# Kernel optimization log

Hardware: AMD Instinct MI355X
Metric: run time of the kernel (lower is better)

The kernel has to match this reference:

```python
import jax, jax.numpy as jnp
import numpy as np

B, N, NH, H = 32, 512, 4, 32      # batch, agents per group, heads, hidden per head
IN_DIM, OUT_DIM = 128, 128
BIG = 9.0e15
SQRT_DK = float(np.sqrt(H))


def setup_inputs() -> dict:
    key = jax.random.key(0)
    keys = iter(jax.random.split(key, 64))

    def nrm(shape, scale=0.05):
        return jax.random.normal(next(keys), shape, dtype=jnp.float32) * scale

    inp = {}
    inp["x0"] = jax.random.normal(next(keys), (B, N, IN_DIM), dtype=jnp.float32)
    inp["x1"] = jax.random.normal(next(keys), (B, N, IN_DIM), dtype=jnp.float32)
    for name in ("m00", "m01", "m10", "m11"):
        inp[name] = jax.random.randint(next(keys), (B, N, N), 0, 2, dtype=jnp.int32)
    # per-group q/k/v projections: Linear(in_dim, NH*H)
    for g in (0, 1):
        inp[f"wq{g}"] = nrm((IN_DIM, NH * H)); inp[f"bq{g}"] = nrm((NH * H,))
        inp[f"wk{g}"] = nrm((IN_DIM, NH * H)); inp[f"bk{g}"] = nrm((NH * H,))
        inp[f"wv{g}"] = nrm((IN_DIM, NH * H)); inp[f"bv{g}"] = nrm((NH * H,))
    # fc_outs[i][j]: Linear(NH*H, H)
    for i in (0, 1):
        for j in (0, 1):
            inp[f"wo{i}{j}"] = nrm((NH * H, H)); inp[f"bo{i}{j}"] = nrm((H,))
    # fc_out_final[i]: Linear(H * 2, out_dim)
    for g in (0, 1):
        inp[f"wf{g}"] = nrm((2 * H, OUT_DIM)); inp[f"bf{g}"] = nrm((OUT_DIM,))
    return inp


def _qkv(x, wq, bq, wk, bk, wv, bv):
    q = jax.nn.relu(x @ wq + bq)
    k = jax.nn.relu(x @ wk + bk)
    v = jax.nn.relu(x @ wv + bv)
    return q, k, v


def _split_heads(t):
    # [B, N, NH*H] -> [B, NH, N, H]; contiguous H-blocks == torch per-head slices
    return t.reshape(B, t.shape[1], NH, H).transpose(0, 2, 1, 3)


def _attend(q, k, v, mask, gate):
    qh, kh, vh = _split_heads(q), _split_heads(k), _split_heads(v)
    logits = jnp.einsum('bhqd,bhkd->bhqk', qh, kh) / SQRT_DK
    m = mask.astype(logits.dtype)[:, None]            # [B,1,Nq,Nk]
    w = jax.nn.softmax(logits * m - BIG * (1.0 - m), axis=-1)
    if gate:
        has = (mask.sum(axis=-1) > 0).astype(w.dtype)  # [B,Nq]
        w = w * has[:, None, :, None]
    out = jnp.einsum('bhqk,bhkd->bhqd', w, vh)
    # heads concatenated along feature dim (matches torch.cat of head slices)
    return out.transpose(0, 2, 1, 3).reshape(B, q.shape[1], NH * H)


def reference(x0, x1, m00, m01, m10, m11,
              wq0, bq0, wk0, bk0, wv0, bv0,
              wq1, bq1, wk1, bk1, wv1, bv1,
              wo00, bo00, wo01, bo01, wo10, bo10, wo11, bo11,
              wf0, bf0, wf1, bf1):
    q0, k0, v0 = _qkv(x0, wq0, bq0, wk0, bk0, wv0, bv0)
    q1, k1, v1 = _qkv(x1, wq1, bq1, wk1, bk1, wv1, bv1)
    inner0 = jax.nn.relu(_attend(q0, k0, v0, m00, gate=False) @ wo00 + bo00)
    inner1 = jax.nn.relu(_attend(q1, k1, v1, m11, gate=False) @ wo11 + bo11)
    inter0 = jax.nn.relu(_attend(q0, k1, v1, m01, gate=True) @ wo01 + bo01)
    inter1 = jax.nn.relu(_attend(q1, k0, v0, m10, gate=True) @ wo10 + bo10)
    out0 = jnp.concatenate([inner0, inter0], axis=-1) @ wf0 + bf0
    out1 = jnp.concatenate([inner1, inter1], axis=-1) @ wf1 + bf1
    return (out0, out1)
```

## Files before the change

### kernel.cpp

```cpp
#include <hip/hip_runtime.h>

#define B_    32
#define N_    512
#define D_    128
#define ROWS  (B_ * N_)
#define SCALE_ 0.17677669529663687f

typedef __bf16 bf16x8 __attribute__((ext_vector_type(8)));
typedef __bf16 bf16x4 __attribute__((ext_vector_type(4)));
typedef float  f32x4  __attribute__((ext_vector_type(4)));

static __device__ __forceinline__ f32x4 mfma16(bf16x8 a, bf16x8 b, f32x4 c) {
  return __builtin_amdgcn_mfma_f32_16x16x32_bf16(a, b, c, 0, 0, 0);
}

__global__ __launch_bounds__(256) void prep_kernel(
    const int* __restrict__ m00, const int* __restrict__ m01,
    const int* __restrict__ m10, const int* __restrict__ m11,
    const float* __restrict__ wq0, const float* __restrict__ wk0, const float* __restrict__ wv0,
    const float* __restrict__ wq1, const float* __restrict__ wk1, const float* __restrict__ wv1,
    const float* __restrict__ wo00, const float* __restrict__ wo01,
    const float* __restrict__ wo10, const float* __restrict__ wo11,
    const float* __restrict__ wf0, const float* __restrict__ wf1,
    __bf16* __restrict__ wtb, __bf16* __restrict__ wob, __bf16* __restrict__ wfb,
    unsigned long long* __restrict__ mpk)
{
  const int bx = blockIdx.x, t = threadIdx.x;
  if (bx < 2048) {
    const int wid = bx * 4 + (t >> 6);
    const int lane = t & 63;
    const int rg = wid & 7, ch = (wid >> 3) & 7, b = (wid >> 6) & 31, a = wid >> 11;
    const int* msel = (a == 0) ? m00 : (a == 1) ? m11 : (a == 2) ? m01 : m10;
    const int* src = msel + ((size_t)b * N_ + rg * 64) * N_ + ch * 64 + lane;
    unsigned long long mine = 0;
    #pragma unroll 8
    for (int it = 0; it < 64; ++it) {
      int v = src[(size_t)it * N_];
      unsigned long long bits = __ballot(v != 0);
      if (it == lane) mine = bits;
    }
    mpk[((size_t)(a * 32 + b) * 8 + ch) * 512 + rg * 64 + lane] = mine;
  } else if (bx < 2054) {
    const int mat = bx - 2048;
    const float* w = (mat == 0) ? wq0 : (mat == 1) ? wk0 : (mat == 2) ? wv0
                   : (mat == 3) ? wq1 : (mat == 4) ? wk1 : wv1;
    __bf16* dst = wtb + mat * 16384;
    for (int idx = t; idx < 16384; idx += 256) {
      const int k = idx >> 7, n = idx & 127;
      dst[n * 128 + k] = (__bf16)w[idx];
    }
  } else if (bx < 2058) {
    const int i = bx - 2054;
    const float* w = (i == 0) ? wo00 : (i == 1) ? wo11 : (i == 2) ? wo01 : wo10;
    __bf16* dst = wob + i * 4096;
    for (int idx = t; idx < 4096; idx += 256) {
      const int k = idx >> 5, n = idx & 31;
      dst[n * 128 + k] = (__bf16)w[idx];
    }
  } else {
    const int g = bx - 2058;
    const float* w = g ? wf1 : wf0;
    __bf16* dst = wfb + g * 8192;
    for (int idx = t; idx < 8192; idx += 256) {
      const int n = idx >> 6, k = idx & 63;
      dst[n * 64 + k] = (__bf16)w[(size_t)k * 128 + n];
    }
  }
}

__global__ __launch_bounds__(256) void qkv_kernel(
    const float* __restrict__ x0, const float* __restrict__ x1,
    const float* __restrict__ bq0, const float* __restrict__ bk0, const float* __restrict__ bv0,
    const float* __restrict__ bq1, const float* __restrict__ bk1, const float* __restrict__ bv1,
    const __bf16* __restrict__ wtb, __bf16* __restrict__ qkvb)
{
  __shared__ __align__(16) __bf16 vtile[128][72];
  const int bx = blockIdx.x;
  const int g = bx >> 8, tile = bx & 255, R0 = tile * 64;
  const int t = threadIdx.x, lane = t & 63, wave = t >> 6;
  const int quad = lane >> 4, ln = lane & 15;
  const float* xs = g ? x1 : x0;

  bf16x8 af[4];
  {
    const int row = R0 + wave * 16 + ln;
    #pragma unroll
    for (int ks = 0; ks < 4; ++ks) {
      const float4* xp = (const float4*)(xs + (size_t)row * D_ + ks * 32 + quad * 8);
      float4 a = xp[0], b = xp[1];
      bf16x8 v;
      v[0] = (__bf16)a.x; v[1] = (__bf16)a.y; v[2] = (__bf16)a.z; v[3] = (__bf16)a.w;
      v[4] = (__bf16)b.x; v[5] = (__bf16)b.y; v[6] = (__bf16)b.z; v[7] = (__bf16)b.w;
      af[ks] = v;
    }
  }
  const f32x4 zero4 = {0.f, 0.f, 0.f, 0.f};

  for (int m = 0; m < 3; ++m) {
    const __bf16* wt = wtb + (g * 3 + m) * 16384;
    const float* bias = (g == 0) ? ((m == 0) ? bq0 : (m == 1) ? bk0 : bv0)
                                 : ((m == 0) ? bq1 : (m == 1) ? bk1 : bv1);
    __bf16* outp = qkvb + (size_t)(g * 3 + m) * (ROWS * D_);

    f32x4 acc[8];
    #pragma unroll
    for (int nt = 0; nt < 8; ++nt) acc[nt] = zero4;
    #pragma unroll
    for (int ks = 0; ks < 4; ++ks) {
      #pragma unroll
      for (int nt = 0; nt < 8; ++nt) {
        bf16x8 bfrag = *(const bf16x8*)(wt + (size_t)(nt * 16 + ln) * D_ + ks * 32 + quad * 8);
        acc[nt] = mfma16(af[ks], bfrag, acc[nt]);
      }
    }

    if (m != 2) {
      const float sc = (m == 0) ? SCALE_ : 1.0f;
      #pragma unroll
      for (int nt = 0; nt < 8; ++nt) {
        const int col = nt * 16 + ln;
        const float bv = bias[col];
        #pragma unroll
        for (int r = 0; r < 4; ++r) {
          float v = fmaxf(acc[nt][r] + bv, 0.f) * sc;
          outp[(size_t)(R0 + wave * 16 + quad * 4 + r) * D_ + col] = (__bf16)v;
        }
      }
    } else {
      #pragma unroll
      for (int nt = 0; nt < 8; ++nt) {
        const int col = nt * 16 + ln;
        const float bv = bias[col];
        #pragma unroll
        for (int r = 0; r < 4; ++r) {
          float v = fmaxf(acc[nt][r] + bv, 0.f);
          vtile[col][wave * 16 + quad * 4 + r] = (__bf16)v;
        }
      }
      __syncthreads();
      const int b = R0 >> 9, kb2 = R0 & 511;
      const int dim = t >> 1, off = (t & 1) * 32;
      uint4* dst = (uint4*)(outp + (size_t)b * (D_ * N_) + (size_t)dim * N_ + kb2 + off);
      const uint4* srcp = (const uint4*)&vtile[dim][off];
      #pragma unroll
      for (int i = 0; i < 4; ++i) dst[i] = srcp[i];
      __syncthreads();
    }
  }
}

__global__ __launch_bounds__(256, 2) void attn_kernel(
    const __bf16* __restrict__ qkvb,
    const unsigned long long* __restrict__ mpk,
    const __bf16* __restrict__ wob,
    const float* __restrict__ bo00, const float* __restrict__ bo01,
    const float* __restrict__ bo10, const float* __restrict__ bo11,
    __bf16* __restrict__ projb)
{
  __shared__ __align__(16) __bf16 raw[18432];

  const int bx = blockIdx.x;
  const int qt = bx >> 7, cb = bx & 127, a = cb >> 5, b = cb & 31;
  const int t = threadIdx.x, lane = t & 63, h = t >> 6;
  const int quad = lane >> 4, ln = lane & 15;

  const int qg = (a == 1 || a == 3) ? 1 : 0;
  const int kg = (a == 1 || a == 2) ? 1 : 0;
  const float* bo = (a == 0) ? bo00 : (a == 1) ? bo11 : (a == 2) ? bo01 : bo10;

  const __bf16* qb  = qkvb + (size_t)(qg * 3 + 0) * (ROWS * D_) + (size_t)(b * N_ + qt * 64) * D_;
  const __bf16* kb  = qkvb + (size_t)(kg * 3 + 1) * (ROWS * D_) + (size_t)b * N_ * D_;
  const __bf16* vtb = qkvb + (size_t)(kg * 3 + 2) * (ROWS * D_) + (size_t)b * D_ * N_;
  const unsigned long long* mrow = mpk + (size_t)(a * 32 + b) * 8 * 512 + qt * 64;

  __bf16* PT = raw + h * 4608;

  bf16x8 qf[4];
  #pragma unroll
  for (int bt = 0; bt < 4; ++bt)
    qf[bt] = *(const bf16x8*)(qb + (size_t)(bt * 16 + ln) * D_ + h * 32 + quad * 8);

  const f32x4 zero4 = {0.f, 0.f, 0.f, 0.f};
  f32x4 Oacc[2][4];
  float lp[4];
  #pragma unroll
  for (int bt = 0; bt < 4; ++bt) {
    lp[bt] = 0.f;
    Oacc[0][bt] = zero4; Oacc[1][bt] = zero4;
  }

  for (int ch = 0; ch < 8; ++ch) {
    const int kc = ch * 64;

    unsigned long long mb[4];
    #pragma unroll
    for (int bt = 0; bt < 4; ++bt)
      mb[bt] = mrow[(size_t)ch * 512 + bt * 16 + ln];

    #pragma unroll
    for (int at = 0; at < 4; ++at) {
      bf16x8 kf = *(const bf16x8*)(kb + (size_t)(kc + at * 16 + ln) * D_ + h * 32 + quad * 8);
      #pragma unroll
      for (int bt = 0; bt < 4; ++bt) {
        f32x4 s = mfma16(kf, qf[bt], zero4);
        bf16x4 pv;
        float ps = 0.f;
        #pragma unroll
        for (int r = 0; r < 4; ++r) {
          const int bit = (int)((mb[bt] >> (at * 16 + quad * 4 + r)) & 1ull);
          const float p = bit ? __expf(s[r]) : 0.f;
          ps += p;
          pv[r] = (__bf16)p;
        }
        lp[bt] += ps;
        *(bf16x4*)&PT[(bt * 16 + ln) * 72 + at * 16 + quad * 4] = pv;
      }
    }

    #pragma unroll
    for (int s2 = 0; s2 < 2; ++s2) {
      bf16x8 pb[4];
      #pragma unroll
      for (int bt = 0; bt < 4; ++bt)
        pb[bt] = *(const bf16x8*)&PT[(bt * 16 + ln) * 72 + s2 * 32 + quad * 8];
      #pragma unroll
      for (int d = 0; d < 2; ++d) {
        bf16x8 vf = *(const bf16x8*)(vtb + (size_t)(h * 32 + d * 16 + ln) * N_ + kc + s2 * 32 + quad * 8);
        #pragma unroll
        for (int bt = 0; bt < 4; ++bt)
          Oacc[d][bt] = mfma16(vf, pb[bt], Oacc[d][bt]);
      }
    }
  }

  float fac[4];
  #pragma unroll
  for (int bt = 0; bt < 4; ++bt) {
    float l = lp[bt] + __shfl_xor(lp[bt], 16);
    l += __shfl_xor(l, 32);
    fac[bt] = (l > 0.f) ? 1.f / l : 0.f;
  }

  __syncthreads();
  __bf16* OL = raw;
  #pragma unroll
  for (int d = 0; d < 2; ++d)
    #pragma unroll
    for (int bt = 0; bt < 4; ++bt) {
      bf16x4 ov;
      #pragma unroll
      for (int r = 0; r < 4; ++r) ov[r] = (__bf16)(Oacc[d][bt][r] * fac[bt]);
      *(bf16x4*)&OL[(bt * 16 + ln) * 136 + h * 32 + d * 16 + quad * 4] = ov;
    }
  __syncthreads();

  const __bf16* wo = wob + a * 4096;
  f32x4 pacc[2];
  pacc[0] = zero4; pacc[1] = zero4;
  #pragma unroll
  for (int ks = 0; ks < 4; ++ks) {
    bf16x8 afr = *(const bf16x8*)&OL[(h * 16 + ln) * 136 + ks * 32 + quad * 8];
    #pragma unroll
    for (int ct = 0; ct < 2; ++ct) {
      bf16x8 bw = *(const bf16x8*)(wo + (size_t)(ct * 16 + ln) * D_ + ks * 32 + quad * 8);
      pacc[ct] = mfma16(afr, bw, pacc[ct]);
    }
  }
  const int R0g = b * N_ + qt * 64;
  #pragma unroll
  for (int ct = 0; ct < 2; ++ct) {
    const int col = ct * 16 + ln;
    const float bv = bo[col];
    #pragma unroll
    for (int r = 0; r < 4; ++r) {
      const float v = fmaxf(pacc[ct][r] + bv, 0.f);
      projb[(size_t)(a * ROWS + R0g + h * 16 + quad * 4 + r) * 32 + col] = (__bf16)v;
    }
  }
}

__global__ __launch_bounds__(256) void outproj_kernel(
    const __bf16* __restrict__ projb, const __bf16* __restrict__ wfb,
    const float* __restrict__ bf0, const float* __restrict__ bf1,
    float* __restrict__ out)
{
  const int t = threadIdx.x, lane = t & 63, w = t >> 6;
  const int quad = lane >> 4, ln = lane & 15;
  const int row = blockIdx.x * 64 + w * 16;
  const f32x4 zero4 = {0.f, 0.f, 0.f, 0.f};

  #pragma unroll
  for (int g = 0; g < 2; ++g) {
    const float* bfp = g ? bf1 : bf0;
    f32x4 acc[8];
    #pragma unroll
    for (int ct = 0; ct < 8; ++ct) acc[ct] = zero4;
    #pragma unroll
    for (int s = 0; s < 2; ++s) {
      const int asrc = s ? (2 + g) : g;
      bf16x8 afr = *(const bf16x8*)(projb + (size_t)(asrc * ROWS + row + ln) * 32 + quad * 8);
      const __bf16* wb = wfb + g * 8192 + s * 32;
      #pragma unroll
      for (int ct = 0; ct < 8; ++ct) {
        bf16x8 bw = *(const bf16x8*)(wb + (size_t)(ct * 16 + ln) * 64 + quad * 8);
        acc[ct] = mfma16(afr, bw, acc[ct]);
      }
    }
    float* og = out + (size_t)g * (ROWS * D_);
    #pragma unroll
    for (int ct = 0; ct < 8; ++ct) {
      const int col = ct * 16 + ln;
      const float bv = bfp[col];
      #pragma unroll
      for (int r = 0; r < 4; ++r)
        og[(size_t)(row + quad * 4 + r) * D_ + col] = acc[ct][r] + bv;
    }
  }
}

extern "C" void kernel_launch(void* const* d_in, const int* in_sizes, int n_in,
                              void* d_out, int out_size, void* d_ws, size_t ws_size,
                              hipStream_t stream)
{
  const float* x0 = (const float*)d_in[0];
  const float* x1 = (const float*)d_in[1];
  const int* m00 = (const int*)d_in[2];
  const int* m01 = (const int*)d_in[3];
  const int* m10 = (const int*)d_in[4];
  const int* m11 = (const int*)d_in[5];
  const float* wq0 = (const float*)d_in[6];  const float* bq0 = (const float*)d_in[7];
  const float* wk0 = (const float*)d_in[8];  const float* bk0 = (const float*)d_in[9];
  const float* wv0 = (const float*)d_in[10]; const float* bv0 = (const float*)d_in[11];
  const float* wq1 = (const float*)d_in[12]; const float* bq1 = (const float*)d_in[13];
  const float* wk1 = (const float*)d_in[14]; const float* bk1 = (const float*)d_in[15];
  const float* wv1 = (const float*)d_in[16]; const float* bv1 = (const float*)d_in[17];
  const float* wo00 = (const float*)d_in[18]; const float* bo00 = (const float*)d_in[19];
  const float* wo01 = (const float*)d_in[20]; const float* bo01 = (const float*)d_in[21];
  const float* wo10 = (const float*)d_in[22]; const float* bo10 = (const float*)d_in[23];
  const float* wo11 = (const float*)d_in[24]; const float* bo11 = (const float*)d_in[25];
  const float* wf0 = (const float*)d_in[26]; const float* bf0 = (const float*)d_in[27];
  const float* wf1 = (const float*)d_in[28]; const float* bf1 = (const float*)d_in[29];

  __bf16* qkvb = (__bf16*)d_ws;
  __bf16* projb = (__bf16*)((char*)d_ws + 25165824);
  __bf16* wtb  = (__bf16*)((char*)d_ws + 29360128);
  __bf16* wob  = (__bf16*)((char*)d_ws + 29556736);
  __bf16* wfb  = (__bf16*)((char*)d_ws + 29589504);
  unsigned long long* mpk = (unsigned long long*)((char*)d_ws + 29622272);

  prep_kernel<<<dim3(2060), dim3(256), 0, stream>>>(
      m00, m01, m10, m11, wq0, wk0, wv0, wq1, wk1, wv1,
      wo00, wo01, wo10, wo11, wf0, wf1, wtb, wob, wfb, mpk);
  qkv_kernel<<<dim3(512), dim3(256), 0, stream>>>(
      x0, x1, bq0, bk0, bv0, bq1, bk1, bv1, wtb, qkvb);
  attn_kernel<<<dim3(1024), dim3(256), 0, stream>>>(
      qkvb, mpk, wob, bo00, bo01, bo10, bo11, projb);
  outproj_kernel<<<dim3(256), dim3(256), 0, stream>>>(
      projb, wfb, bf0, bf1, (float*)d_out);
}
```

Measured before the change: 328.8 us.

## Rework mask packing, parallelize weight prep, use exp2 and prefetch masks

The mask bit-packing now assigns one wave per mask row and reads it with coalesced loads, eight ballots per row instead of strided column reads. Weight conversion is spread over many more blocks with float4 loads. The log2(e) factor is folded into the Q scale so the softmax can use the hardware exp2, and the mask words for the next key chunk are prefetched in the attention loop. A trailing __syncthreads in the QKV kernel is removed, which appears safe because each block writes the V tile only once.

```diff
diff --git a/kernel.cpp b/kernel.cpp
--- a/kernel.cpp
+++ b/kernel.cpp
@@ -4,7 +4,7 @@
 #define N_    512
 #define D_    128
 #define ROWS  (B_ * N_)
-#define SCALE_ 0.17677669529663687f
+#define SCALE2_ (0.17677669529663687f * 1.4426950408889634f)
 
 typedef __bf16 bf16x8 __attribute__((ext_vector_type(8)));
 typedef __bf16 bf16x4 __attribute__((ext_vector_type(4)));
@@ -26,45 +26,54 @@
     unsigned long long* __restrict__ mpk)
 {
   const int bx = blockIdx.x, t = threadIdx.x;
-  if (bx < 2048) {
+  if (bx < 16384) {
     const int wid = bx * 4 + (t >> 6);
     const int lane = t & 63;
-    const int rg = wid & 7, ch = (wid >> 3) & 7, b = (wid >> 6) & 31, a = wid >> 11;
+    const int row = wid & 511, b = (wid >> 9) & 31, a = wid >> 14;
     const int* msel = (a == 0) ? m00 : (a == 1) ? m11 : (a == 2) ? m01 : m10;
-    const int* src = msel + ((size_t)b * N_ + rg * 64) * N_ + ch * 64 + lane;
+    const int* src = msel + ((size_t)b * N_ + row) * N_;
     unsigned long long mine = 0;
-    #pragma unroll 8
-    for (int it = 0; it < 64; ++it) {
-      int v = src[(size_t)it * N_];
-      unsigned long long bits = __ballot(v != 0);
-      if (it == lane) mine = bits;
-    }
-    mpk[((size_t)(a * 32 + b) * 8 + ch) * 512 + rg * 64 + lane] = mine;
-  } else if (bx < 2054) {
-    const int mat = bx - 2048;
+    #pragma unroll
+    for (int ch = 0; ch < 8; ++ch) {
+      const int v = src[ch * 64 + lane];
+      const unsigned long long bits = __ballot(v != 0);
+      if (lane == ch) mine = bits;
+    }
+    if (lane < 8)
+      mpk[((size_t)(a * 32 + b) * 8 + lane) * 512 + row] = mine;
+  } else if (bx < 16480) {
+    const int i = bx - 16384, mat = i >> 4, sub = i & 15;
     const float* w = (mat == 0) ? wq0 : (mat == 1) ? wk0 : (mat == 2) ? wv0
                    : (mat == 3) ? wq1 : (mat == 4) ? wk1 : wv1;
     __bf16* dst = wtb + mat * 16384;
-    for (int idx = t; idx < 16384; idx += 256) {
-      const int k = idx >> 7, n = idx & 127;
-      dst[n * 128 + k] = (__bf16)w[idx];
-    }
-  } else if (bx < 2058) {
-    const int i = bx - 2054;
-    const float* w = (i == 0) ? wo00 : (i == 1) ? wo11 : (i == 2) ? wo01 : wo10;
-    __bf16* dst = wob + i * 4096;
-    for (int idx = t; idx < 4096; idx += 256) {
-      const int k = idx >> 5, n = idx & 31;
-      dst[n * 128 + k] = (__bf16)w[idx];
-    }
+    const int fidx = sub * 256 + t;
+    const float4 f = ((const float4*)w)[fidx];
+    const int e = fidx * 4, k = e >> 7, n = e & 127;
+    dst[(n + 0) * 128 + k] = (__bf16)f.x;
+    dst[(n + 1) * 128 + k] = (__bf16)f.y;
+    dst[(n + 2) * 128 + k] = (__bf16)f.z;
+    dst[(n + 3) * 128 + k] = (__bf16)f.w;
+  } else if (bx < 16496) {
+    const int i = bx - 16480, a = i >> 2, sub = i & 3;
+    const float* w = (a == 0) ? wo00 : (a == 1) ? wo11 : (a == 2) ? wo01 : wo10;
+    __bf16* dst = wob + a * 4096;
+    const int fidx = sub * 256 + t;
+    const float4 f = ((const float4*)w)[fidx];
+    const int e = fidx * 4, k = e >> 5, n = e & 31;
+    dst[(n + 0) * 128 + k] = (__bf16)f.x;
+    dst[(n + 1) * 128 + k] = (__bf16)f.y;
+    dst[(n + 2) * 128 + k] = (__bf16)f.z;
+    dst[(n + 3) * 128 + k] = (__bf16)f.w;
   } else {
-    const int g = bx - 2058;
+    const int i = bx - 16496, g = i >> 3, sub = i & 7;
     const float* w = g ? wf1 : wf0;
     __bf16* dst = wfb + g * 8192;
-    for (int idx = t; idx < 8192; idx += 256) {
-      const int n = idx >> 6, k = idx & 63;
-      dst[n * 64 + k] = (__bf16)w[(size_t)k * 128 + n];
-    }
+    const int d0 = sub * 1024 + t * 4;
+    const int n = d0 >> 6, k = d0 & 63;
+    bf16x4 v;
+    #pragma unroll
+    for (int j = 0; j < 4; ++j) v[j] = (__bf16)w[(size_t)(k + j) * 128 + n];
+    *(bf16x4*)&dst[d0] = v;
   }
 }
 
@@ -115,7 +124,7 @@
     }
 
     if (m != 2) {
-      const float sc = (m == 0) ? SCALE_ : 1.0f;
+      const float sc = (m == 0) ? SCALE2_ : 1.0f;
       #pragma unroll
       for (int nt = 0; nt < 8; ++nt) {
         const int col = nt * 16 + ln;
@@ -144,7 +153,6 @@
       const uint4* srcp = (const uint4*)&vtile[dim][off];
       #pragma unroll
       for (int i = 0; i < 4; ++i) dst[i] = srcp[i];
-      __syncthreads();
     }
   }
 }
@@ -189,13 +197,19 @@
     Oacc[0][bt] = zero4; Oacc[1][bt] = zero4;
   }
 
+  unsigned long long mb[4];
+  #pragma unroll
+  for (int bt = 0; bt < 4; ++bt) mb[bt] = mrow[bt * 16 + ln];
+
   for (int ch = 0; ch < 8; ++ch) {
     const int kc = ch * 64;
 
-    unsigned long long mb[4];
-    #pragma unroll
-    for (int bt = 0; bt < 4; ++bt)
-      mb[bt] = mrow[(size_t)ch * 512 + bt * 16 + ln];
+    unsigned long long mbn[4] = {0, 0, 0, 0};
+    if (ch < 7) {
+      #pragma unroll
+      for (int bt = 0; bt < 4; ++bt)
+        mbn[bt] = mrow[(size_t)(ch + 1) * 512 + bt * 16 + ln];
+    }
 
     #pragma unroll
     for (int at = 0; at < 4; ++at) {
@@ -208,7 +222,7 @@
         #pragma unroll
         for (int r = 0; r < 4; ++r) {
           const int bit = (int)((mb[bt] >> (at * 16 + quad * 4 + r)) & 1ull);
-          const float p = bit ? __expf(s[r]) : 0.f;
+          const float p = bit ? __builtin_amdgcn_exp2f(s[r]) : 0.f;
           ps += p;
           pv[r] = (__bf16)p;
         }
@@ -231,6 +245,9 @@
           Oacc[d][bt] = mfma16(vf, pb[bt], Oacc[d][bt]);
       }
     }
+
+    #pragma unroll
+    for (int bt = 0; bt < 4; ++bt) mb[bt] = mbn[bt];
   }
 
   float fac[4];
@@ -348,7 +365,7 @@
   __bf16* wfb  = (__bf16*)((char*)d_ws + 29589504);
   unsigned long long* mpk = (unsigned long long*)((char*)d_ws + 29622272);
 
-  prep_kernel<<<dim3(2060), dim3(256), 0, stream>>>(
+  prep_kernel<<<dim3(16512), dim3(256), 0, stream>>>(
       m00, m01, m10, m11, wq0, wk0, wv0, wq1, wk1, wv1,
       wo00, wo01, wo10, wo11, wf0, wf1, wtb, wob, wfb, mpk);
   qkv_kernel<<<dim3(512), dim3(256), 0, stream>>>(
```

Measured after the change: 302.2 us. -8.1%, faster.
